# Performance work log

Hardware: AMD Instinct MI355X
Metric: run time of the kernel (lower is better)

Reference implementation:

```python
import jax, jax.numpy as jnp
import numpy as np
from jax import lax

B = 2
H = W = 128          # resolution
N = H * W            # 16384 tokens
C = 128              # in_channels
C2 = C // 2          # 64, attention dim
G = 16               # window_size
HEADS = 8
HDIM = C2 // HEADS   # 8
EPS = 1e-5
DN = ('NCHW', 'OIHW', 'NCHW')


def setup_inputs():
    key = jax.random.key(0)
    ks = jax.random.split(key, 16)
    r = lambda i, shape, s=0.02: jax.random.normal(ks[i], shape, jnp.float32) * s
    z = lambda shape: jnp.zeros(shape, jnp.float32)
    o = lambda shape: jnp.ones(shape, jnp.float32)
    return {
        'x_C': jax.random.normal(ks[0], (B, N, C), jnp.float32),
        'x_T': jax.random.normal(ks[1], (B, N, C), jnp.float32),
        # S_conv = depthwise 3x3 + pointwise 1x1
        'conv1_dw': r(2, (C, 1, 3, 3)), 'conv1_dw_b': z((C,)),
        'conv1_pw': r(3, (C, C, 1, 1)), 'conv1_pw_b': z((C,)),
        'bn1_gamma': o((C,)), 'bn1_beta': z((C,)),
        'bn1_mean': r(4, (C,), 0.1), 'bn1_var': jnp.abs(r(5, (C,), 0.1)) + 1.0,
        'enc_W': r(6, (C, C2)), 'enc_b': z((C2,)),
        'pos': r(7, (1, N, C2)),
        'ln_gamma': o((C2,)), 'ln_beta': z((C2,)),
        'qkv_W': r(8, (C2, 3 * C2)),                      # qkv_bias=False
        'proj_W': r(9, (C2, C2)), 'proj_b': z((C2,)),
        'ffn_W1': r(10, (C2, C2)), 'ffn_b1': z((C2,)),
        'ffn_W2': r(11, (C2, C2)), 'ffn_b2': z((C2,)),
        'dec_W': r(12, (C2, C)), 'dec_b': z((C,)),
    }


def _ln(x, g, b):
    m = jnp.mean(x, -1, keepdims=True)
    v = jnp.var(x, -1, keepdims=True)
    return (x - m) * jax.lax.rsqrt(v + EPS) * g + b


def _win_part(x):  # (B,N,C2) -> (B*nW, G*G, C2)
    x = x.reshape(B, H // G, G, W // G, G, C2).transpose(0, 1, 3, 2, 4, 5)
    return x.reshape(-1, G * G, C2)


def _win_rev(x):  # (B*nW, G*G, C2) -> (B,N,C2)
    x = x.reshape(B, H // G, W // G, G, G, C2).transpose(0, 1, 3, 2, 4, 5)
    return x.reshape(B, N, C2)


def reference(x_C, x_T, conv1_dw, conv1_dw_b, conv1_pw, conv1_pw_b,
              bn1_gamma, bn1_beta, bn1_mean, bn1_var,
              enc_W, enc_b, pos, ln_gamma, ln_beta, qkv_W,
              proj_W, proj_b, ffn_W1, ffn_b1, ffn_W2, ffn_b2, dec_W, dec_b):
    cb = lambda a: a[None, :, None, None]
    # ---- CNN branch on x_C: S_conv -> BN(eval) -> ReLU, residual
    xC = x_C.reshape(B, H, W, C).transpose(0, 3, 1, 2)  # NCHW
    h = lax.conv_general_dilated(xC, conv1_dw, (1, 1), 'SAME',
                                 feature_group_count=C, dimension_numbers=DN) + cb(conv1_dw_b)
    h = lax.conv_general_dilated(h, conv1_pw, (1, 1), 'SAME',
                                 dimension_numbers=DN) + cb(conv1_pw_b)
    h = (h - cb(bn1_mean)) * cb(bn1_gamma * jax.lax.rsqrt(bn1_var + EPS)) + cb(bn1_beta)
    x1 = jax.nn.relu(h) + xC
    # ---- x_T branch: source overwrites conv/bn outputs -> x2 = relu(x_T) + x_T
    xT = x_T.reshape(B, H, W, C).transpose(0, 3, 1, 2)
    x2 = jax.nn.relu(xT) + xT
    # ---- flatten to tokens, encode + positional embedding
    x = x1.transpose(0, 2, 3, 1).reshape(B, N, C)
    y = x2.transpose(0, 2, 3, 1).reshape(B, N, C)
    x_poi = x @ enc_W + enc_b + pos
    y_poi = y @ enc_W + enc_b + pos
    # ---- window partition + LayerNorm
    wx = _ln(_win_part(x_poi), ln_gamma, ln_beta)
    wy = _ln(_win_part(y_poi), ln_gamma, ln_beta)
    # ---- dual-stream windowed attention (cross values)
    scale = HDIM ** -0.5
    def qkv(t):
        q, k, v = jnp.split(t @ qkv_W, 3, axis=-1)
        re = lambda a: a.reshape(-1, G * G, HEADS, HDIM).transpose(0, 2, 1, 3)
        return re(q), re(k), re(v)
    q, k, v = qkv(wx)
    q1, k1, v1 = qkv(wy)
    attn = jax.nn.softmax(jnp.einsum('bhid,bhjd->bhij', q * scale, k), axis=-1)
    attn1 = jax.nn.softmax(jnp.einsum('bhid,bhjd->bhij', q1 * scale, k1), axis=-1)
    ox = jnp.einsum('bhij,bhjd->bhid', attn, v1).transpose(0, 2, 1, 3).reshape(-1, G * G, C2)
    oy = jnp.einsum('bhij,bhjd->bhid', attn1, v).transpose(0, 2, 1, 3).reshape(-1, G * G, C2)
    ox = ox @ proj_W + proj_b + wx
    oy = oy @ proj_W + proj_b + wy
    # ---- window reverse + FFN (pre-LN, residual)
    x = _win_rev(ox)
    y = _win_rev(oy)
    ffn = lambda t: jax.nn.relu(_ln(t, ln_gamma, ln_beta) @ ffn_W1 + ffn_b1) @ ffn_W2 + ffn_b2
    x = x + ffn(x)
    y = y + ffn(y)
    # ---- decode back to C channels; to_3d(reshape) is identity on (B,N,C)
    return (x @ dec_W + dec_b) + (y @ dec_W + dec_b)
```

## Files before the change

### kernel.cpp

```cpp
#include <hip/hip_runtime.h>
#include <hip/hip_bf16.h>
#include <math.h>

#define EPSF 1e-5f
#define KSCL 0.51010090329771713f

#if __has_builtin(__builtin_amdgcn_exp2f)
#define EXP2(x) __builtin_amdgcn_exp2f(x)
#else
#define EXP2(x) exp2f(x)
#endif

typedef __attribute__((ext_vector_type(8))) short short8;
typedef __attribute__((ext_vector_type(16))) float f32x16;

__device__ __forceinline__ float bf2f(unsigned short u) {
    union { unsigned int i; float f; } x; x.i = ((unsigned int)u) << 16; return x.f;
}
__device__ __forceinline__ unsigned int f2bf(float f) {
    union { float f; unsigned int i; } u; u.f = f;
    unsigned int r = u.i + 0x7FFFu + ((u.i >> 16) & 1u);
    return r >> 16;
}
__device__ __forceinline__ unsigned cvtpk(float a, float b) {
    unsigned r;
    asm("v_cvt_pk_bf16_f32 %0, %1, %2" : "=v"(r) : "v"(a), "v"(b));
    return r;
}
__device__ __forceinline__ void bbuild(const unsigned pk[8], int lh,
                                       short8& B0, short8& B1) {
    unsigned xs[8];
    #pragma unroll
    for (int i = 0; i < 8; ++i) xs[i] = (unsigned)__shfl_xor((int)pk[i], 32);
    uint4 w0, w1;
    w0.x = lh ? xs[2] : pk[0]; w0.y = lh ? xs[3] : pk[1];
    w0.z = lh ? pk[2] : xs[0]; w0.w = lh ? pk[3] : xs[1];
    w1.x = lh ? xs[6] : pk[4]; w1.y = lh ? xs[7] : pk[5];
    w1.z = lh ? pk[6] : xs[4]; w1.w = lh ? pk[7] : xs[5];
    B0 = __builtin_bit_cast(short8, w0);
    B1 = __builtin_bit_cast(short8, w1);
}

__global__ __launch_bounds__(256) void k_dwconv(
    const float* __restrict__ xC, const float* __restrict__ dwW,
    const float* __restrict__ dwB, unsigned short* __restrict__ xdwb,
    const float* __restrict__ qkvW, const float* __restrict__ pw,
    const float* __restrict__ pwb, const float* __restrict__ gam,
    const float* __restrict__ bet, const float* __restrict__ mean,
    const float* __restrict__ var, const float* __restrict__ projW,
    const float* __restrict__ W1, const float* __restrict__ W2,
    const float* __restrict__ decW, const float* __restrict__ encW,
    unsigned short* __restrict__ qkvWT, unsigned short* __restrict__ weff,
    float* __restrict__ beff, unsigned short* __restrict__ projWTn,
    unsigned short* __restrict__ W1Tn, unsigned short* __restrict__ W2Tn,
    unsigned short* __restrict__ decTn, unsigned short* __restrict__ encWTn)
{
    int tid = threadIdx.x;
    int bid = blockIdx.x;
    if (bid >= 1024) {
        int pid = (bid - 1024) * 256 + tid;
        if (pid < 12288) {
            int o = pid >> 6, c = pid & 63;
            qkvWT[pid] = (unsigned short)f2bf(qkvW[c * 192 + o]);
        } else if (pid < 28672) {
            int i = pid - 12288;
            int co = i >> 7;
            float sc = gam[co] * rsqrtf(var[co] + EPSF);
            weff[i] = (unsigned short)f2bf(pw[i] * sc);
        } else if (pid < 32768) {
            int i = pid - 28672, m = i >> 6, c = i & 63;
            projWTn[i] = (unsigned short)f2bf(projW[c * 64 + m]);
        } else if (pid < 36864) {
            int i = pid - 32768, m = i >> 6, c = i & 63;
            W1Tn[i] = (unsigned short)f2bf(W1[c * 64 + m]);
        } else if (pid < 40960) {
            int i = pid - 36864, m = i >> 6, c = i & 63;
            W2Tn[i] = (unsigned short)f2bf(W2[c * 64 + m]);
        } else if (pid < 49152) {
            int i = pid - 40960, m = i >> 6, c = i & 63;
            decTn[i] = (unsigned short)f2bf(decW[c * 128 + m]);
        } else if (pid < 57344) {
            int i = pid - 49152, m = i >> 7, c = i & 127;
            encWTn[i] = (unsigned short)f2bf(encW[c * 64 + m]);
        } else if (pid < 57472) {
            int i = pid - 57344;
            float sc = gam[i] * rsqrtf(var[i] + EPSF);
            beff[i] = (pwb[i] - mean[i]) * sc + bet[i];
        }
        return;
    }
    __shared__ float s_w[128 * 9];
    __shared__ float s_bias[128];
    for (int i = tid; i < 128 * 9; i += 256) s_w[i] = dwW[i];
    if (tid < 128) s_bias[tid] = dwB[tid];
    __syncthreads();
    int idx = bid * 256 + tid;
    int c4 = (idx & 31) * 4;
    int pg = idx >> 5;
    int t0 = pg * 4;
    int b = t0 >> 14, n = t0 & 16383;
    int row = n >> 7, col0 = n & 127;
    float vb[3][6][4];
    #pragma unroll
    for (int ky = 0; ky < 3; ++ky) {
        int r = row + ky - 1;
        #pragma unroll
        for (int cx = 0; cx < 6; ++cx) {
            int cl = col0 + cx - 1;
            if ((unsigned)r < 128u && (unsigned)cl < 128u) {
                *(float4*)&vb[ky][cx][0] =
                    *(const float4*)&xC[((size_t)(b << 14) + (r << 7) + cl) * 128 + c4];
            } else {
                vb[ky][cx][0] = 0.f; vb[ky][cx][1] = 0.f; vb[ky][cx][2] = 0.f; vb[ky][cx][3] = 0.f;
            }
        }
    }
    float acc[4][4];
    #pragma unroll
    for (int p = 0; p < 4; ++p)
        #pragma unroll
        for (int j = 0; j < 4; ++j) acc[p][j] = s_bias[c4 + j];
    #pragma unroll
    for (int ky = 0; ky < 3; ++ky)
        #pragma unroll
        for (int kx = 0; kx < 3; ++kx)
            #pragma unroll
            for (int j = 0; j < 4; ++j) {
                float w = s_w[(c4 + j) * 9 + ky * 3 + kx];
                #pragma unroll
                for (int p = 0; p < 4; ++p)
                    acc[p][j] = fmaf(w, vb[ky][p + kx][j], acc[p][j]);
            }
    #pragma unroll
    for (int p = 0; p < 4; ++p) {
        uint2 o;
        o.x = f2bf(acc[p][0]) | (f2bf(acc[p][1]) << 16);
        o.y = f2bf(acc[p][2]) | (f2bf(acc[p][3]) << 16);
        *(uint2*)&xdwb[((size_t)t0 + p) * 128 + c4] = o;
    }
}

__global__ __launch_bounds__(256) void k_pw(
    const unsigned short* __restrict__ xdwb, const float* __restrict__ xC,
    const unsigned short* __restrict__ weff, const float* __restrict__ beff,
    unsigned short* __restrict__ x1b)
{
    int tid = threadIdx.x;
    int wv = tid >> 6, lane = tid & 63, l31 = lane & 31, lh = lane >> 5;
    int wr = wv >> 1, wc = wv & 1;
    int T0 = blockIdx.x * 64;
    int ta = T0 + wr * 32 + l31;
    short8 af[8];
    #pragma unroll
    for (int ks = 0; ks < 8; ++ks)
        af[ks] = *(const short8*)&xdwb[(size_t)ta * 128 + ks * 16 + lh * 8];
    #pragma unroll
    for (int nt = 0; nt < 2; ++nt) {
        int co = wc * 64 + nt * 32 + l31;
        f32x16 acc = {};
        #pragma unroll
        for (int ks = 0; ks < 8; ++ks) {
            short8 bfr = *(const short8*)&weff[(size_t)co * 128 + ks * 16 + lh * 8];
            acc = __builtin_amdgcn_mfma_f32_32x32x16_bf16(af[ks], bfr, acc, 0, 0, 0);
        }
        float be = beff[co];
        #pragma unroll
        for (int r = 0; r < 16; ++r) {
            int tt = T0 + wr * 32 + (r & 3) + 8 * (r >> 2) + 4 * lh;
            float v = fmaxf(acc[r] + be, 0.f) + xC[(size_t)tt * 128 + co];
            x1b[(size_t)tt * 128 + co] = (unsigned short)f2bf(v);
        }
    }
}

__global__ __launch_bounds__(256) void k_enc(
    const unsigned short* __restrict__ x1b, const float* __restrict__ xT,
    const unsigned short* __restrict__ encWTn, const float* __restrict__ encb,
    const float* __restrict__ pos, const float* __restrict__ lng,
    const float* __restrict__ lnb,
    unsigned short* __restrict__ wxb, unsigned short* __restrict__ wyb)
{
    int tid = threadIdx.x;
    int wv = tid >> 6, l31 = tid & 31, lh = (tid >> 5) & 1;
    int s = blockIdx.y;
    int t = blockIdx.x * 128 + wv * 32 + l31;
    int n = t & 16383;
    short8 bf[8];
    if (s == 0) {
        #pragma unroll
        for (int ks = 0; ks < 8; ++ks)
            bf[ks] = *(const short8*)&x1b[(size_t)t * 128 + ks * 16 + lh * 8];
    } else {
        #pragma unroll
        for (int ks = 0; ks < 8; ++ks) {
            float4 f0 = *(const float4*)&xT[(size_t)t * 128 + ks * 16 + lh * 8];
            float4 f1 = *(const float4*)&xT[(size_t)t * 128 + ks * 16 + lh * 8 + 4];
            float r0 = f0.x > 0.f ? 2.f * f0.x : f0.x;
            float r1 = f0.y > 0.f ? 2.f * f0.y : f0.y;
            float r2 = f0.z > 0.f ? 2.f * f0.z : f0.z;
            float r3 = f0.w > 0.f ? 2.f * f0.w : f0.w;
            float r4 = f1.x > 0.f ? 2.f * f1.x : f1.x;
            float r5 = f1.y > 0.f ? 2.f * f1.y : f1.y;
            float r6 = f1.z > 0.f ? 2.f * f1.z : f1.z;
            float r7 = f1.w > 0.f ? 2.f * f1.w : f1.w;
            uint4 w;
            w.x = cvtpk(r0, r1); w.y = cvtpk(r2, r3);
            w.z = cvtpk(r4, r5); w.w = cvtpk(r6, r7);
            bf[ks] = __builtin_bit_cast(short8, w);
        }
    }
    f32x16 xm[2];
    #pragma unroll
    for (int ta = 0; ta < 2; ++ta) {
        f32x16 acc = {};
        #pragma unroll
        for (int ks = 0; ks < 8; ++ks) {
            short8 af = *(const short8*)&encWTn[(size_t)(ta * 32 + l31) * 128 + ks * 16 + lh * 8];
            acc = __builtin_amdgcn_mfma_f32_32x32x16_bf16(af, bf[ks], acc, 0, 0, 0);
        }
        #pragma unroll
        for (int g = 0; g < 4; ++g) {
            int c0 = ta * 32 + g * 8 + lh * 4;
            float4 eb = *(const float4*)&encb[c0];
            float4 pv = *(const float4*)&pos[(size_t)n * 64 + c0];
            acc[g * 4 + 0] += eb.x + pv.x;
            acc[g * 4 + 1] += eb.y + pv.y;
            acc[g * 4 + 2] += eb.z + pv.z;
            acc[g * 4 + 3] += eb.w + pv.w;
        }
        xm[ta] = acc;
    }
    float sm = 0.f, sq = 0.f;
    #pragma unroll
    for (int ta = 0; ta < 2; ++ta)
        #pragma unroll
        for (int r = 0; r < 16; ++r) { float v = xm[ta][r]; sm += v; sq += v * v; }
    sm += __shfl_xor(sm, 32); sq += __shfl_xor(sq, 32);
    float mu = sm * (1.f / 64.f);
    float rs = rsqrtf(fmaxf(sq * (1.f / 64.f) - mu * mu, 0.f) + EPSF);
    unsigned short* dstb = s ? wyb : wxb;
    #pragma unroll
    for (int ta = 0; ta < 2; ++ta)
        #pragma unroll
        for (int g = 0; g < 4; ++g) {
            int c0 = ta * 32 + g * 8 + lh * 4;
            float4 gg = *(const float4*)&lng[c0];
            float4 bb = *(const float4*)&lnb[c0];
            float u0 = (xm[ta][g * 4 + 0] - mu) * rs * gg.x + bb.x;
            float u1 = (xm[ta][g * 4 + 1] - mu) * rs * gg.y + bb.y;
            float u2 = (xm[ta][g * 4 + 2] - mu) * rs * gg.z + bb.z;
            float u3 = (xm[ta][g * 4 + 3] - mu) * rs * gg.w + bb.w;
            uint2 o; o.x = cvtpk(u0, u1); o.y = cvtpk(u2, u3);
            *(uint2*)&dstb[(size_t)t * 64 + c0] = o;
        }
}

__global__ __launch_bounds__(256) void k_qkv(
    const unsigned short* __restrict__ wxb, const unsigned short* __restrict__ wyb,
    const unsigned short* __restrict__ qkvWT,
    unsigned short* __restrict__ qk, unsigned short* __restrict__ vT)
{
    int tid = threadIdx.x;
    int wv = tid >> 6, lane = tid & 63, l31 = lane & 31, lh = lane >> 5;
    int s = blockIdx.y;
    int T0 = blockIdx.x * 128;
    int b = T0 >> 14;
    int row = (T0 & 16383) >> 7;
    const unsigned short* src = s ? wyb : wxb;
    int t = T0 + wv * 32 + l31;
    short8 bfr[4];
    #pragma unroll
    for (int ks = 0; ks < 4; ++ks)
        bfr[ks] = *(const short8*)&src[(size_t)t * 64 + ks * 16 + lh * 8];
    int cp = wv * 32 + l31;
    int wid = ((row >> 4) << 3) + (cp >> 4);
    int p = ((row & 15) << 4) + (cp & 15);
    size_t cb = (size_t)(s * 2 + b) * 512 + wid;
    #pragma unroll
    for (int nt = 0; nt < 6; ++nt) {
        f32x16 acc = {};
        #pragma unroll
        for (int ks = 0; ks < 4; ++ks) {
            short8 afr = *(const short8*)&qkvWT[(size_t)(nt * 32 + l31) * 64 + ks * 16 + lh * 8];
            acc = __builtin_amdgcn_mfma_f32_32x32x16_bf16(afr, bfr[ks], acc, 0, 0, 0);
        }
        if (nt < 4) {
            const float scl = nt < 2 ? 1.f : KSCL;
            const int sec = nt < 2 ? 0 : 1;
            #pragma unroll
            for (int g = 0; g < 4; ++g) {
                int head = (nt & 1) * 4 + g;
                unsigned short* rec = qk + (cb + head * 64) * 4096;
                float f0 = acc[4 * g + 0] * scl, f1 = acc[4 * g + 1] * scl;
                float f2 = acc[4 * g + 2] * scl, f3 = acc[4 * g + 3] * scl;
                unsigned u01 = cvtpk(f0, f1), u23 = cvtpk(f2, f3);
                int off = p * 16 + sec * 8 + 4 * lh;
                *(unsigned*)(rec + off) = u01;
                *(unsigned*)(rec + off + 2) = u23;
            }
        } else {
            #pragma unroll
            for (int g = 0; g < 4; ++g) {
                int head = (nt - 4) * 4 + g;
                unsigned short* vrec = vT + (cb + head * 64) * 2048;
                int d0 = 4 * lh;
                vrec[(d0 + 0) * 256 + p] = (unsigned short)f2bf(acc[4 * g + 0]);
                vrec[(d0 + 1) * 256 + p] = (unsigned short)f2bf(acc[4 * g + 1]);
                vrec[(d0 + 2) * 256 + p] = (unsigned short)f2bf(acc[4 * g + 2]);
                vrec[(d0 + 3) * 256 + p] = (unsigned short)f2bf(acc[4 * g + 3]);
            }
        }
    }
}

__global__ __launch_bounds__(256) void k_attn(
    const unsigned short* __restrict__ qk, const unsigned short* __restrict__ vT,
    float* __restrict__ ox, float* __restrict__ oy)
{
    int tid = threadIdx.x;
    int wave = tid >> 6, lane = tid & 63;
    int lh = lane >> 5, l31 = lane & 31;
    int bx = blockIdx.x;
    int s = bx >> 10;
    int r = bx & 1023;
    int head = (r >> 6) & 7, wid = r & 63, b = r >> 9;
    const unsigned short* qbase = qk + ((size_t)s * 1024 + r) * 4096;
    const unsigned short* vbase = vT + ((size_t)(s ^ 1) * 1024 + r) * 2048;

    short8 qf[2];
    #pragma unroll
    for (int qt = 0; qt < 2; ++qt) {
        uint4 v = {0u, 0u, 0u, 0u};
        if (lh == 0) v = *(const uint4*)(qbase + (size_t)(wave * 64 + qt * 32 + l31) * 16);
        qf[qt] = __builtin_bit_cast(short8, v);
    }
    f32x16 acc[2];
    #pragma unroll
    for (int qt = 0; qt < 2; ++qt) acc[qt] = (f32x16){};
    const unsigned ONES = 0x3F803F80u;

    for (int jt = 0; jt < 8; ++jt) {
        uint4 kv = {0u, 0u, 0u, 0u};
        if (lh == 0) kv = *(const uint4*)(qbase + (size_t)(jt * 32 + l31) * 16 + 8);
        short8 kf = __builtin_bit_cast(short8, kv);
        uint2 a0 = {ONES, ONES}, a1 = {ONES, ONES}, a2 = {ONES, ONES}, a3 = {ONES, ONES};
        if (l31 < 8) {
            const unsigned short* vp = vbase + l31 * 256 + jt * 32 + lh * 4;
            a0 = *(const uint2*)vp;
            a1 = *(const uint2*)(vp + 8);
            a2 = *(const uint2*)(vp + 16);
            a3 = *(const uint2*)(vp + 24);
        }
        uint4 vaw = {a0.x, a0.y, a1.x, a1.y};
        uint4 vbw = {a2.x, a2.y, a3.x, a3.y};
        short8 vf0 = __builtin_bit_cast(short8, vaw);
        short8 vf1 = __builtin_bit_cast(short8, vbw);
        #pragma unroll
        for (int qt = 0; qt < 2; ++qt) {
            f32x16 c = __builtin_amdgcn_mfma_f32_32x32x16_bf16(kf, qf[qt], (f32x16){}, 0, 0, 0);
            float p[16];
            #pragma unroll
            for (int i = 0; i < 16; ++i) p[i] = EXP2(c[i]);
            unsigned pk[8];
            #pragma unroll
            for (int i = 0; i < 8; ++i) pk[i] = cvtpk(p[2 * i], p[2 * i + 1]);
            uint4 bw0 = {pk[0], pk[1], pk[2], pk[3]};
            uint4 bw1 = {pk[4], pk[5], pk[6], pk[7]};
            short8 B0 = __builtin_bit_cast(short8, bw0);
            short8 B1 = __builtin_bit_cast(short8, bw1);
            acc[qt] = __builtin_amdgcn_mfma_f32_32x32x16_bf16(vf0, B0, acc[qt], 0, 0, 0);
            acc[qt] = __builtin_amdgcn_mfma_f32_32x32x16_bf16(vf1, B1, acc[qt], 0, 0, 0);
        }
    }
    float* dst = s ? oy : ox;
    #pragma unroll
    for (int qt = 0; qt < 2; ++qt) {
        float inv = 1.f / acc[qt][4];
        int p = wave * 64 + qt * 32 + l31;
        int orow = (wid >> 3) * 16 + (p >> 4);
        int ocol = (wid & 7) * 16 + (p & 15);
        size_t t = (size_t)b * 16384 + orow * 128 + ocol;
        float4 o;
        o.x = acc[qt][0] * inv; o.y = acc[qt][1] * inv;
        o.z = acc[qt][2] * inv; o.w = acc[qt][3] * inv;
        *(float4*)&dst[t * 64 + head * 8 + lh * 4] = o;
    }
}

__global__ __launch_bounds__(256) void k_fusedec(
    const float* __restrict__ ox, const float* __restrict__ oy,
    const unsigned short* __restrict__ wxb, const unsigned short* __restrict__ wyb,
    const unsigned short* __restrict__ projWTn, const float* __restrict__ projb,
    const unsigned short* __restrict__ W1Tn, const float* __restrict__ b1,
    const unsigned short* __restrict__ W2Tn, const float* __restrict__ b2,
    const unsigned short* __restrict__ decTn, const float* __restrict__ decb,
    const float* __restrict__ lng, const float* __restrict__ lnb,
    float* __restrict__ out)
{
    int tid = threadIdx.x;
    int wv = tid >> 6, l31 = tid & 31, lh = (tid >> 5) & 1;
    int t = blockIdx.x * 128 + wv * 32 + l31;
    f32x16 zacc[2];
    zacc[0] = (f32x16){}; zacc[1] = (f32x16){};
    #pragma unroll 1
    for (int s = 0; s < 2; ++s) {
        const float* osrc = s ? oy : ox;
        const unsigned short* wsrc = s ? wyb : wxb;
        short8 bo[4];
        #pragma unroll
        for (int kap = 0; kap < 4; ++kap) {
            float4 f0 = *(const float4*)&osrc[(size_t)t * 64 + kap * 16 + lh * 8];
            float4 f1 = *(const float4*)&osrc[(size_t)t * 64 + kap * 16 + lh * 8 + 4];
            uint4 w;
            w.x = cvtpk(f0.x, f0.y); w.y = cvtpk(f0.z, f0.w);
            w.z = cvtpk(f1.x, f1.y); w.w = cvtpk(f1.z, f1.w);
            bo[kap] = __builtin_bit_cast(short8, w);
        }
        f32x16 a1[2];
        #pragma unroll
        for (int ta = 0; ta < 2; ++ta) {
            f32x16 acc = {};
            #pragma unroll
            for (int kap = 0; kap < 4; ++kap) {
                short8 af = *(const short8*)&projWTn[(size_t)(ta * 32 + l31) * 64 + kap * 16 + lh * 8];
                acc = __builtin_amdgcn_mfma_f32_32x32x16_bf16(af, bo[kap], acc, 0, 0, 0);
            }
            #pragma unroll
            for (int g = 0; g < 4; ++g) {
                int c0 = ta * 32 + g * 8 + lh * 4;
                float4 pb = *(const float4*)&projb[c0];
                uint2 wr2 = *(const uint2*)&wsrc[(size_t)t * 64 + c0];
                acc[g * 4 + 0] += pb.x + bf2f((unsigned short)(wr2.x & 0xffffu));
                acc[g * 4 + 1] += pb.y + bf2f((unsigned short)(wr2.x >> 16));
                acc[g * 4 + 2] += pb.z + bf2f((unsigned short)(wr2.y & 0xffffu));
                acc[g * 4 + 3] += pb.w + bf2f((unsigned short)(wr2.y >> 16));
            }
            a1[ta] = acc;
        }
        float sm = 0.f, sq = 0.f;
        #pragma unroll
        for (int ta = 0; ta < 2; ++ta)
            #pragma unroll
            for (int r = 0; r < 16; ++r) { float v = a1[ta][r]; sm += v; sq += v * v; }
        sm += __shfl_xor(sm, 32); sq += __shfl_xor(sq, 32);
        float mu = sm * (1.f / 64.f);
        float rs = rsqrtf(fmaxf(sq * (1.f / 64.f) - mu * mu, 0.f) + EPSF);
        unsigned pku[2][8];
        #pragma unroll
        for (int ta = 0; ta < 2; ++ta)
            #pragma unroll
            for (int g = 0; g < 4; ++g) {
                int c0 = ta * 32 + g * 8 + lh * 4;
                float4 gg = *(const float4*)&lng[c0];
                float4 bb = *(const float4*)&lnb[c0];
                float u0 = (a1[ta][g * 4 + 0] - mu) * rs * gg.x + bb.x;
                float u1 = (a1[ta][g * 4 + 1] - mu) * rs * gg.y + bb.y;
                float u2 = (a1[ta][g * 4 + 2] - mu) * rs * gg.z + bb.z;
                float u3 = (a1[ta][g * 4 + 3] - mu) * rs * gg.w + bb.w;
                pku[ta][g * 2]     = cvtpk(u0, u1);
                pku[ta][g * 2 + 1] = cvtpk(u2, u3);
            }
        short8 Bu[4];
        bbuild(pku[0], lh, Bu[0], Bu[1]);
        bbuild(pku[1], lh, Bu[2], Bu[3]);
        unsigned pkh[2][8];
        #pragma unroll
        for (int th = 0; th < 2; ++th) {
            f32x16 acc = {};
            #pragma unroll
            for (int kap = 0; kap < 4; ++kap) {
                short8 af = *(const short8*)&W1Tn[(size_t)(th * 32 + l31) * 64 + kap * 16 + lh * 8];
                acc = __builtin_amdgcn_mfma_f32_32x32x16_bf16(af, Bu[kap], acc, 0, 0, 0);
            }
            #pragma unroll
            for (int g = 0; g < 4; ++g) {
                int c0 = th * 32 + g * 8 + lh * 4;
                float4 bb = *(const float4*)&b1[c0];
                float h0 = fmaxf(acc[g * 4 + 0] + bb.x, 0.f);
                float h1 = fmaxf(acc[g * 4 + 1] + bb.y, 0.f);
                float h2 = fmaxf(acc[g * 4 + 2] + bb.z, 0.f);
                float h3 = fmaxf(acc[g * 4 + 3] + bb.w, 0.f);
                pkh[th][g * 2]     = cvtpk(h0, h1);
                pkh[th][g * 2 + 1] = cvtpk(h2, h3);
            }
        }
        short8 Bh[4];
        bbuild(pkh[0], lh, Bh[0], Bh[1]);
        bbuild(pkh[1], lh, Bh[2], Bh[3]);
        #pragma unroll
        for (int ta = 0; ta < 2; ++ta) {
            f32x16 a3 = a1[ta];
            #pragma unroll
            for (int g = 0; g < 4; ++g) {
                int c0 = ta * 32 + g * 8 + lh * 4;
                float4 bb = *(const float4*)&b2[c0];
                a3[g * 4 + 0] += bb.x; a3[g * 4 + 1] += bb.y;
                a3[g * 4 + 2] += bb.z; a3[g * 4 + 3] += bb.w;
            }
            #pragma unroll
            for (int kap = 0; kap < 4; ++kap) {
                short8 af = *(const short8*)&W2Tn[(size_t)(ta * 32 + l31) * 64 + kap * 16 + lh * 8];
                a3 = __builtin_amdgcn_mfma_f32_32x32x16_bf16(af, Bh[kap], a3, 0, 0, 0);
            }
            zacc[ta] += a3;
        }
    }
    unsigned pkz[2][8];
    #pragma unroll
    for (int ta = 0; ta < 2; ++ta)
        #pragma unroll
        for (int g = 0; g < 4; ++g) {
            pkz[ta][g * 2]     = cvtpk(zacc[ta][g * 4 + 0], zacc[ta][g * 4 + 1]);
            pkz[ta][g * 2 + 1] = cvtpk(zacc[ta][g * 4 + 2], zacc[ta][g * 4 + 3]);
        }
    short8 Bz[4];
    bbuild(pkz[0], lh, Bz[0], Bz[1]);
    bbuild(pkz[1], lh, Bz[2], Bz[3]);
    #pragma unroll
    for (int mu4 = 0; mu4 < 4; ++mu4) {
        f32x16 a4 = {};
        #pragma unroll
        for (int g = 0; g < 4; ++g) {
            int c0 = mu4 * 32 + g * 8 + lh * 4;
            float4 db = *(const float4*)&decb[c0];
            a4[g * 4 + 0] = 2.f * db.x; a4[g * 4 + 1] = 2.f * db.y;
            a4[g * 4 + 2] = 2.f * db.z; a4[g * 4 + 3] = 2.f * db.w;
        }
        #pragma unroll
        for (int kap = 0; kap < 4; ++kap) {
            short8 af = *(const short8*)&decTn[(size_t)(mu4 * 32 + l31) * 64 + kap * 16 + lh * 8];
            a4 = __builtin_amdgcn_mfma_f32_32x32x16_bf16(af, Bz[kap], a4, 0, 0, 0);
        }
        #pragma unroll
        for (int g = 0; g < 4; ++g) {
            int c0 = mu4 * 32 + g * 8 + lh * 4;
            float4 o;
            o.x = a4[g * 4 + 0]; o.y = a4[g * 4 + 1];
            o.z = a4[g * 4 + 2]; o.w = a4[g * 4 + 3];
            *(float4*)&out[(size_t)t * 128 + c0] = o;
        }
    }
}

extern "C" void kernel_launch(void* const* d_in, const int* in_sizes, int n_in,
                              void* d_out, int out_size, void* d_ws, size_t ws_size,
                              hipStream_t stream) {
    const float* x_C   = (const float*)d_in[0];
    const float* x_T   = (const float*)d_in[1];
    const float* dwW   = (const float*)d_in[2];
    const float* dwB   = (const float*)d_in[3];
    const float* pw    = (const float*)d_in[4];
    const float* pwb   = (const float*)d_in[5];
    const float* gam   = (const float*)d_in[6];
    const float* bet   = (const float*)d_in[7];
    const float* mean  = (const float*)d_in[8];
    const float* var   = (const float*)d_in[9];
    const float* encW  = (const float*)d_in[10];
    const float* encb  = (const float*)d_in[11];
    const float* pos   = (const float*)d_in[12];
    const float* lng   = (const float*)d_in[13];
    const float* lnb   = (const float*)d_in[14];
    const float* qkvW  = (const float*)d_in[15];
    const float* projW = (const float*)d_in[16];
    const float* projb = (const float*)d_in[17];
    const float* W1    = (const float*)d_in[18];
    const float* b1    = (const float*)d_in[19];
    const float* W2    = (const float*)d_in[20];
    const float* b2    = (const float*)d_in[21];
    const float* decW  = (const float*)d_in[22];
    const float* decb  = (const float*)d_in[23];
    float* out = (float*)d_out;

    float* ws = (float*)d_ws;
    unsigned short* xdwb = (unsigned short*)ws;
    unsigned short* x1b  = (unsigned short*)(ws + 2097152);
    unsigned short* qkb  = (unsigned short*)(ws + 4194304);
    unsigned short* vTb  = (unsigned short*)(ws + 8388608);
    unsigned short* wxb  = (unsigned short*)(ws + 10485760);
    unsigned short* wyb  = (unsigned short*)(ws + 11534336);
    float* ox   = ws + 12582912;
    float* oy   = ws + 14680064;
    unsigned short* qkvWT   = (unsigned short*)(ws + 16777216);
    unsigned short* weff    = (unsigned short*)(ws + 16783360);
    float*          beff    = ws + 16791552;
    unsigned short* projWTn = (unsigned short*)(ws + 16791680);
    unsigned short* W1Tn    = (unsigned short*)(ws + 16793728);
    unsigned short* W2Tn    = (unsigned short*)(ws + 16795776);
    unsigned short* decTn   = (unsigned short*)(ws + 16797824);
    unsigned short* encWTn  = (unsigned short*)(ws + 16801920);

    k_dwconv<<<1249, 256, 0, stream>>>(x_C, dwW, dwB, xdwb, qkvW, pw, pwb,
                                       gam, bet, mean, var, projW, W1, W2, decW,
                                       encW, qkvWT, weff, beff, projWTn,
                                       W1Tn, W2Tn, decTn, encWTn);
    k_pw<<<512, 256, 0, stream>>>(xdwb, x_C, weff, beff, x1b);
    k_enc<<<dim3(256, 2), 256, 0, stream>>>(x1b, x_T, encWTn, encb, pos,
                                            lng, lnb, wxb, wyb);
    k_qkv<<<dim3(256, 2), 256, 0, stream>>>(wxb, wyb, qkvWT, qkb, vTb);
    k_attn<<<2048, 256, 0, stream>>>(qkb, vTb, ox, oy);
    k_fusedec<<<256, 256, 0, stream>>>(ox, oy, wxb, wyb, projWTn, projb,
                                       W1Tn, b1, W2Tn, b2, decTn, decb,
                                       lng, lnb, out);
}
```

Baseline: 100.8 us.

## Fuse encoder and QKV kernels, store attention output as bf16

```diff
diff --git a/kernel.cpp b/kernel.cpp
--- a/kernel.cpp
+++ b/kernel.cpp
@@ -173,17 +173,19 @@
     }
 }
 
-__global__ __launch_bounds__(256) void k_enc(
+__global__ __launch_bounds__(256) void k_encqkv(
     const unsigned short* __restrict__ x1b, const float* __restrict__ xT,
     const unsigned short* __restrict__ encWTn, const float* __restrict__ encb,
     const float* __restrict__ pos, const float* __restrict__ lng,
-    const float* __restrict__ lnb,
-    unsigned short* __restrict__ wxb, unsigned short* __restrict__ wyb)
+    const float* __restrict__ lnb, const unsigned short* __restrict__ qkvWT,
+    unsigned short* __restrict__ wxb, unsigned short* __restrict__ wyb,
+    unsigned short* __restrict__ qk, unsigned short* __restrict__ vT)
 {
     int tid = threadIdx.x;
     int wv = tid >> 6, l31 = tid & 31, lh = (tid >> 5) & 1;
     int s = blockIdx.y;
-    int t = blockIdx.x * 128 + wv * 32 + l31;
+    int T0 = blockIdx.x * 128;
+    int t = T0 + wv * 32 + l31;
     int n = t & 16383;
     short8 bf[8];
     if (s == 0) {
@@ -239,6 +241,7 @@
     float mu = sm * (1.f / 64.f);
     float rs = rsqrtf(fmaxf(sq * (1.f / 64.f) - mu * mu, 0.f) + EPSF);
     unsigned short* dstb = s ? wyb : wxb;
+    unsigned pku[2][8];
     #pragma unroll
     for (int ta = 0; ta < 2; ++ta)
         #pragma unroll
@@ -250,28 +253,16 @@
             float u1 = (xm[ta][g * 4 + 1] - mu) * rs * gg.y + bb.y;
             float u2 = (xm[ta][g * 4 + 2] - mu) * rs * gg.z + bb.z;
             float u3 = (xm[ta][g * 4 + 3] - mu) * rs * gg.w + bb.w;
-            uint2 o; o.x = cvtpk(u0, u1); o.y = cvtpk(u2, u3);
+            pku[ta][g * 2]     = cvtpk(u0, u1);
+            pku[ta][g * 2 + 1] = cvtpk(u2, u3);
+            uint2 o; o.x = pku[ta][g * 2]; o.y = pku[ta][g * 2 + 1];
             *(uint2*)&dstb[(size_t)t * 64 + c0] = o;
         }
-}
-
-__global__ __launch_bounds__(256) void k_qkv(
-    const unsigned short* __restrict__ wxb, const unsigned short* __restrict__ wyb,
-    const unsigned short* __restrict__ qkvWT,
-    unsigned short* __restrict__ qk, unsigned short* __restrict__ vT)
-{
-    int tid = threadIdx.x;
-    int wv = tid >> 6, lane = tid & 63, l31 = lane & 31, lh = lane >> 5;
-    int s = blockIdx.y;
-    int T0 = blockIdx.x * 128;
+    short8 Bu[4];
+    bbuild(pku[0], lh, Bu[0], Bu[1]);
+    bbuild(pku[1], lh, Bu[2], Bu[3]);
     int b = T0 >> 14;
     int row = (T0 & 16383) >> 7;
-    const unsigned short* src = s ? wyb : wxb;
-    int t = T0 + wv * 32 + l31;
-    short8 bfr[4];
-    #pragma unroll
-    for (int ks = 0; ks < 4; ++ks)
-        bfr[ks] = *(const short8*)&src[(size_t)t * 64 + ks * 16 + lh * 8];
     int cp = wv * 32 + l31;
     int wid = ((row >> 4) << 3) + (cp >> 4);
     int p = ((row & 15) << 4) + (cp & 15);
@@ -282,7 +273,7 @@
         #pragma unroll
         for (int ks = 0; ks < 4; ++ks) {
             short8 afr = *(const short8*)&qkvWT[(size_t)(nt * 32 + l31) * 64 + ks * 16 + lh * 8];
-            acc = __builtin_amdgcn_mfma_f32_32x32x16_bf16(afr, bfr[ks], acc, 0, 0, 0);
+            acc = __builtin_amdgcn_mfma_f32_32x32x16_bf16(afr, Bu[ks], acc, 0, 0, 0);
         }
         if (nt < 4) {
             const float scl = nt < 2 ? 1.f : KSCL;
@@ -315,7 +306,7 @@
 
 __global__ __launch_bounds__(256) void k_attn(
     const unsigned short* __restrict__ qk, const unsigned short* __restrict__ vT,
-    float* __restrict__ ox, float* __restrict__ oy)
+    unsigned short* __restrict__ obx, unsigned short* __restrict__ oby)
 {
     int tid = threadIdx.x;
     int wave = tid >> 6, lane = tid & 63;
@@ -372,7 +363,7 @@
             acc[qt] = __builtin_amdgcn_mfma_f32_32x32x16_bf16(vf1, B1, acc[qt], 0, 0, 0);
         }
     }
-    float* dst = s ? oy : ox;
+    unsigned short* dst = s ? oby : obx;
     #pragma unroll
     for (int qt = 0; qt < 2; ++qt) {
         float inv = 1.f / acc[qt][4];
@@ -380,15 +371,15 @@
         int orow = (wid >> 3) * 16 + (p >> 4);
         int ocol = (wid & 7) * 16 + (p & 15);
         size_t t = (size_t)b * 16384 + orow * 128 + ocol;
-        float4 o;
-        o.x = acc[qt][0] * inv; o.y = acc[qt][1] * inv;
-        o.z = acc[qt][2] * inv; o.w = acc[qt][3] * inv;
-        *(float4*)&dst[t * 64 + head * 8 + lh * 4] = o;
+        uint2 o;
+        o.x = cvtpk(acc[qt][0] * inv, acc[qt][1] * inv);
+        o.y = cvtpk(acc[qt][2] * inv, acc[qt][3] * inv);
+        *(uint2*)&dst[t * 64 + head * 8 + lh * 4] = o;
     }
 }
 
 __global__ __launch_bounds__(256) void k_fusedec(
-    const float* __restrict__ ox, const float* __restrict__ oy,
+    const unsigned short* __restrict__ obx, const unsigned short* __restrict__ oby,
     const unsigned short* __restrict__ wxb, const unsigned short* __restrict__ wyb,
     const unsigned short* __restrict__ projWTn, const float* __restrict__ projb,
     const unsigned short* __restrict__ W1Tn, const float* __restrict__ b1,
@@ -404,18 +395,12 @@
     zacc[0] = (f32x16){}; zacc[1] = (f32x16){};
     #pragma unroll 1
     for (int s = 0; s < 2; ++s) {
-        const float* osrc = s ? oy : ox;
+        const unsigned short* osrc = s ? oby : obx;
         const unsigned short* wsrc = s ? wyb : wxb;
         short8 bo[4];
         #pragma unroll
-        for (int kap = 0; kap < 4; ++kap) {
-            float4 f0 = *(const float4*)&osrc[(size_t)t * 64 + kap * 16 + lh * 8];
-            float4 f1 = *(const float4*)&osrc[(size_t)t * 64 + kap * 16 + lh * 8 + 4];
-            uint4 w;
-            w.x = cvtpk(f0.x, f0.y); w.y = cvtpk(f0.z, f0.w);
-            w.z = cvtpk(f1.x, f1.y); w.w = cvtpk(f1.z, f1.w);
-            bo[kap] = __builtin_bit_cast(short8, w);
-        }
+        for (int kap = 0; kap < 4; ++kap)
+            bo[kap] = *(const short8*)&osrc[(size_t)t * 64 + kap * 16 + lh * 8];
         f32x16 a1[2];
         #pragma unroll
         for (int ta = 0; ta < 2; ++ta) {
@@ -578,8 +563,8 @@
     unsigned short* vTb  = (unsigned short*)(ws + 8388608);
     unsigned short* wxb  = (unsigned short*)(ws + 10485760);
     unsigned short* wyb  = (unsigned short*)(ws + 11534336);
-    float* ox   = ws + 12582912;
-    float* oy   = ws + 14680064;
+    unsigned short* obx  = (unsigned short*)(ws + 12582912);
+    unsigned short* oby  = (unsigned short*)(ws + 13631488);
     unsigned short* qkvWT   = (unsigned short*)(ws + 16777216);
     unsigned short* weff    = (unsigned short*)(ws + 16783360);
     float*          beff    = ws + 16791552;
@@ -594,11 +579,10 @@
                                        encW, qkvWT, weff, beff, projWTn,
                                        W1Tn, W2Tn, decTn, encWTn);
     k_pw<<<512, 256, 0, stream>>>(xdwb, x_C, weff, beff, x1b);
-    k_enc<<<dim3(256, 2), 256, 0, stream>>>(x1b, x_T, encWTn, encb, pos,
-                                            lng, lnb, wxb, wyb);
-    k_qkv<<<dim3(256, 2), 256, 0, stream>>>(wxb, wyb, qkvWT, qkb, vTb);
-    k_attn<<<2048, 256, 0, stream>>>(qkb, vTb, ox, oy);
-    k_fusedec<<<256, 256, 0, stream>>>(ox, oy, wxb, wyb, projWTn, projb,
+    k_encqkv<<<dim3(256, 2), 256, 0, stream>>>(x1b, x_T, encWTn, encb, pos,
+                                               lng, lnb, qkvWT, wxb, wyb, qkb, vTb);
+    k_attn<<<2048, 256, 0, stream>>>(qkb, vTb, obx, oby);
+    k_fusedec<<<256, 256, 0, stream>>>(obx, oby, wxb, wyb, projWTn, projb,
                                        W1Tn, b1, W2Tn, b2, decTn, decb,
                                        lng, lnb, out);
 }
```

New measurement: 95.67 us. -5.1%, faster.
